# Performance work log

Hardware: AMD Instinct MI355X
Metric: run time of the kernel (lower is better)

The kernel has to match this reference:

```python
import jax, jax.numpy as jnp
import numpy as np
from jax import lax

NAMES = ['k', 'v', 'q', 'eta', 'alpha', 'memory']
RES = {'k': True, 'v': True, 'q': True, 'eta': False, 'alpha': False, 'memory': True}
CHUNK = 16


def _mlp(x, st, residual):
    # x: (B,C,d_in); st W1:(B,d_out,d_hid) W2:(B,d_hid,d_in) b1:(B,d_out) b2:(B,d_hid)
    h = jax.nn.silu(jnp.einsum('bcd,bhd->bch', x, st['W2']) + st['b2'][:, None, :])
    out = jnp.einsum('bch,boh->bco', h, st['W1']) + st['b1'][:, None, :]
    return x + out if residual else out


def _dgd_grads(x, target, st, residual):
    # manual chain rule for L = (1/2C)||M(x)-target||^2
    C = x.shape[1]
    pre = jnp.einsum('bcd,bhd->bch', x, st['W2']) + st['b2'][:, None, :]
    sig = jax.nn.sigmoid(pre)
    h = pre * sig  # silu
    pred = jnp.einsum('bch,boh->bco', h, st['W1']) + st['b1'][:, None, :]
    if residual:
        pred = x + pred
    error = (pred - target) / C  # (B,C,d_out)
    dW1 = jnp.einsum('bco,bch->boh', error, h)
    db1 = error.sum(axis=1)
    dl_dh = jnp.einsum('bco,boh->bch', error, st['W1'])
    silu_grad = sig * (1.0 + pre * (1.0 - sig))
    dl_dpre = dl_dh * silu_grad
    dW2 = jnp.einsum('bch,bcd->bhd', dl_dpre, x)
    db2 = dl_dpre.sum(axis=1)
    return {'W1': dW1, 'W2': dW2, 'b1': db1, 'b2': db2}


def _clamp(w):
    B = w.shape[0]
    flat = w.reshape(B, -1)
    norm = jnp.linalg.norm(flat, axis=1)
    max_n = np.sqrt(flat.shape[1]).astype(np.float32)
    scale = jnp.minimum(max_n / (norm + 1e-8), 1.0)
    return w * scale.reshape((B,) + (1,) * (w.ndim - 1))


def _l2norm(x):
    return x / jnp.maximum(jnp.linalg.norm(x, axis=-1, keepdims=True), 1e-12)


def _titans(x, mods, in_W, in_b, out_W, out_b, ln_g, ln_b):
    B, T, _ = x.shape
    C = CHUNK
    NC = T // C
    z = x @ in_W.T + in_b  # (B,T,d_memory)
    zc = z.reshape(B, NC, C, -1).transpose(1, 0, 2, 3)  # (NC,B,C,d)

    states = {}
    for name in NAMES:
        W1, b1, W2, b2 = mods[name]
        states[name] = {
            'W1': jnp.broadcast_to(W1, (B,) + W1.shape),
            'b1': jnp.broadcast_to(b1, (B,) + b1.shape),
            'W2': jnp.broadcast_to(W2, (B,) + W2.shape),
            'b2': jnp.broadcast_to(b2, (B,) + b2.shape),
        }

    def step(st, z_chunk):
        k = _mlp(z_chunk, st['k'], True)
        v = _mlp(z_chunk, st['v'], True)
        q = _mlp(z_chunk, st['q'], True)
        eta = jax.nn.sigmoid(_mlp(z_chunk, st['eta'], False))    # (B,C,1)
        alpha = jax.nn.sigmoid(_mlp(z_chunk, st['alpha'], False))
        k = _l2norm(k)
        q = _l2norm(q)
        o = _mlp(q, st['memory'], True)
        ea = eta.mean(axis=1)    # (B,1)
        aa = alpha.mean(axis=1)  # (B,1)
        new = {}
        for name in NAMES:
            s = st[name]
            res = RES[name]
            v_hat = lax.stop_gradient(_mlp(v, s, res))
            g = _dgd_grads(k, v_hat, s, res)
            ns = {}
            for pn in ('W1', 'W2', 'b1', 'b2'):
                gr = g[pn]
                a = aa.reshape((aa.shape[0],) + (1,) * (gr.ndim - 1))
                e = ea.reshape((ea.shape[0],) + (1,) * (gr.ndim - 1))
                ns[pn] = _clamp(a * s[pn] - e * gr)
            new[name] = ns
        new = jax.tree.map(lax.stop_gradient, new)  # bptt_depth=0 detach
        return new, o

    _, outs = lax.scan(step, states, zc)  # outs: (NC,B,C,d)
    out = outs.transpose(1, 0, 2, 3).reshape(B, T, -1)
    mu = out.mean(axis=-1, keepdims=True)
    var = out.var(axis=-1, keepdims=True)
    out = (out - mu) / jnp.sqrt(var + 1e-5) * ln_g + ln_b
    return out @ out_W.T + out_b


def setup_inputs() -> dict:
    key = jax.random.key(0)
    B, T, Dm = 4, 2048, 1024
    Dmem = 1024
    ks = jax.random.split(key, 10)
    inp = {'x': jax.random.normal(ks[0], (B, T, Dm), jnp.float32)}
    d_outs = {'k': Dmem, 'v': Dmem, 'q': Dmem, 'eta': 1, 'alpha': 1, 'memory': Dmem}
    b1_special = {'eta': -3.0, 'alpha': 3.0}
    for i, (m, do) in enumerate(d_outs.items()):
        inp[f'{m}_W1'] = jnp.zeros((do, Dmem), jnp.float32)
        inp[f'{m}_b1'] = jnp.full((do,), b1_special.get(m, 0.0), jnp.float32)
        inp[f'{m}_W2'] = (jax.random.normal(ks[1 + i], (Dmem, Dm), jnp.float32)
                          * np.sqrt(2.0 / Dm).astype(np.float32))
        inp[f'{m}_b2'] = jnp.zeros((Dmem,), jnp.float32)
    inp['in_W'] = jax.random.normal(ks[7], (Dmem, Dm), jnp.float32) * 0.02
    inp['in_b'] = jnp.zeros((Dmem,), jnp.float32)
    inp['out_W'] = jax.random.normal(ks[8], (Dm, Dmem), jnp.float32) * 0.02
    inp['out_b'] = jnp.zeros((Dm,), jnp.float32)
    inp['ln_g'] = jnp.ones((Dmem,), jnp.float32)
    inp['ln_b'] = jnp.zeros((Dmem,), jnp.float32)
    return inp


def reference(x, k_W1, k_b1, k_W2, k_b2, v_W1, v_b1, v_W2, v_b2,
              q_W1, q_b1, q_W2, q_b2, eta_W1, eta_b1, eta_W2, eta_b2,
              alpha_W1, alpha_b1, alpha_W2, alpha_b2,
              memory_W1, memory_b1, memory_W2, memory_b2,
              in_W, in_b, out_W, out_b, ln_g, ln_b):
    mods = {
        'k': (k_W1, k_b1, k_W2, k_b2),
        'v': (v_W1, v_b1, v_W2, v_b2),
        'q': (q_W1, q_b1, q_W2, q_b2),
        'eta': (eta_W1, eta_b1, eta_W2, eta_b2),
        'alpha': (alpha_W1, alpha_b1, alpha_W2, alpha_b2),
        'memory': (memory_W1, memory_b1, memory_W2, memory_b2),
    }
    return _titans(x, mods, in_W, in_b, out_W, out_b, ln_g, ln_b)
```

## Files before the change

### kernel.cpp

```cpp
#include <hip/hip_runtime.h>
#include <math.h>

#define DI __device__ __forceinline__

namespace {

typedef unsigned short u16;
typedef unsigned int u32;
typedef __attribute__((ext_vector_type(8))) short bf8;
typedef __attribute__((ext_vector_type(4))) float f4;

DI f4 MFB(bf8 a, bf8 b, f4 c) { return __builtin_amdgcn_mfma_f32_16x16x32_bf16(a, b, c, 0, 0, 0); }

constexpr int DOUTS[6] = {1024, 1024, 1024, 1, 1, 1024};
constexpr int BIGM[4] = {0, 1, 2, 5};

constexpr long SZ_BIGM = 2100224, SZ_SMALLM = 1051648;
constexpr long MODOFF[6] = {0, SZ_BIGM, 2 * SZ_BIGM, 3 * SZ_BIGM,
                            3 * SZ_BIGM + SZ_SMALLM, 3 * SZ_BIGM + 2 * SZ_SMALLM};
constexpr long BSTRIDE = 3 * SZ_BIGM + 2 * SZ_SMALLM + SZ_BIGM;

constexpr long OFF_Z     = 0;
constexpr long OFF_STATE = 8388608;
constexpr long OFF_SPRE5 = OFF_STATE + 4 * BSTRIDE;
// ... 37 lines not shown
}

DI void sumsqReduce(float ss, float* slack, float* dst) {
#pragma unroll
  for (int st = 32; st >= 1; st >>= 1) ss += __shfl_xor(ss, st);
  const int tid = threadIdx.x;
  if ((tid & 63) == 0) slack[tid >> 6] = ss;
  __syncthreads();
  if (tid == 0) atomicAdd(dst, slack[0] + slack[1] + slack[2] + slack[3]);
  __syncthreads();
}

DI void split3v(const float v[8], bf8& p0, bf8& p1, bf8& p2) {
#pragma unroll
  for (int i = 0; i < 8; i++) {
    const u32 u = __float_as_uint(v[i]);
    const float f0 = __uint_as_float(u & 0xffff0000u);
    const float r1 = v[i] - f0;
    const u32 u1 = __float_as_uint(r1);
    const float f1 = __uint_as_float(u1 & 0xffff0000u);
    const float r2 = r1 - f1;
    p0[i] = (short)(u >> 16);
    p1[i] = (short)(u1 >> 16);
    p2[i] = (short)f2bf(r2);
  }
}
DI void split3p(const float* p, bf8& p0, bf8& p1, bf8& p2) {
  const float4 a = *(const float4*)p, b = *(const float4*)(p + 4);
  const float v[8] = {a.x, a.y, a.z, a.w, b.x, b.y, b.z, b.w};
  split3v(v, p0, p1, p2);
}

__global__ void k_probe(float* ws) {
  const int l = threadIdx.x, cl = l & 15, kq = l >> 4;
  bf8 af, bf_;
#pragma unroll
  for (int i = 0; i < 8; i++) { af[i] = 0; bf_[i] = 0; }
  if (kq == 0) {
    af[0] = (short)f2bf((float)(cl + 1));
    bf_[0] = (short)f2bf((float)(128 * (cl + 1)));
  }
  f4 d = MFB(af, bf_, f4{0.f, 0.f, 0.f, 0.f});
  bool m0 = true, m1 = true;
#pragma unroll
  for (int r = 0; r < 4; r++) {
    m0 = m0 && (d[r] == (float)((kq * 4 + r + 1) * 128 * (cl + 1)));
    m1 = m1 && (d[r] == (float)((cl + 1) * 128 * (kq * 4 + r + 1)));
  }
  const unsigned long long b0 = __ballot(m0), b1 = __ballot(m1);
  if (l == 0) ws[OFF_FLAG] = (b0 == ~0ull) ? 0.f : ((b1 == ~0ull) ? 1.f : 0.f);
}

template <class EF>
DI void mcK1(float* sm, const float* __restrict__ X, const float* W,
             int n0, int flg, EF&& ef) {
  const int tid = threadIdx.x, g = tid >> 6, l = tid & 63, cl = l & 15, kq = l >> 4;
  f4 a0 = {0.f, 0.f, 0.f, 0.f}, a1 = {0.f, 0.f, 0.f, 0.f};
  const float* Xr = X + (long)cl * 1024 + g * 256 + kq * 8;
  const float* Wr0 = W + (long)(n0 + cl) * 1024 + g * 256 + kq * 8;
  const float* Wr1 = Wr0 + 16 * 1024;
#pragma unroll 2
  for (int ch = 0; ch < 8; ch++) {
    bf8 x0, x1, x2, w0, w1, w2;
    split3p(Xr + ch * 32, x0, x1, x2);
    split3p(Wr0 + ch * 32, w0, w1, w2);
    a0 = MFB(x2, w0, a0); a0 = MFB(x1, w1, a0); a0 = MFB(x0, w2, a0);
    a0 = MFB(x1, w0, a0); a0 = MFB(x0, w1, a0); a0 = MFB(x0, w0, a0);
    split3p(Wr1 + ch * 32, w0, w1, w2);
    a1 = MFB(x2, w0, a1); a1 = MFB(x1, w1, a1); a1 = MFB(x0, w2, a1);
    a1 = MFB(x1, w0, a1); a1 = MFB(x0, w1, a1); a1 = MFB(x0, w0, a1);
  }
  *(f4*)(sm + g * 256 + l * 4) = a0;
  *(f4*)(sm + 1024 + g * 256 + l * 4) = a1;
  __syncthreads();
  const int le = tid >> 2, re = tid & 3;
  const int ccl = le & 15, ckq = le >> 4;
  const int c = flg ? ccl : ckq * 4 + re;
  const int nb = flg ? ckq * 4 + re : ccl;
#pragma unroll
  for (int half = 0; half < 2; half++) {
    const float v = sm[half * 1024 + le * 4 + re] + sm[half * 1024 + 256 + le * 4 + re] +
                    sm[half * 1024 + 512 + le * 4 + re] + sm[half * 1024 + 768 + le * 4 + re];
    ef(c, n0 + half * 16 + nb, v);
  }
}

template <class EF>
DI void mcK2(float* sm, const float* __restrict__ X1, const float* __restrict__ X2,
             const float* W, int n0, int flg, EF&& ef) {
  const int tid = threadIdx.x, g = tid >> 6, l = tid & 63, cl = l & 15, kq = l >> 4;
  f4 a10 = {0.f, 0.f, 0.f, 0.f}, a11 = {0.f, 0.f, 0.f, 0.f};
  f4 a20 = {0.f, 0.f, 0.f, 0.f}, a21 = {0.f, 0.f, 0.f, 0.f};
  const float* X1r = X1 + (long)cl * 1024 + g * 256 + kq * 8;
  const float* X2r = X2 + (long)cl * 1024 + g * 256 + kq * 8;
  const float* Wr0 = W + (long)(n0 + cl) * 1024 + g * 256 + kq * 8;
  const float* Wr1 = Wr0 + 16 * 1024;
#pragma unroll 2
  for (int ch = 0; ch < 8; ch++) {
    bf8 x0, x1, x2, y0, y1, y2, w0, w1, w2;
    split3p(X1r + ch * 32, x0, x1, x2);
    split3p(X2r + ch * 32, y0, y1, y2);
    split3p(Wr0 + ch * 32, w0, w1, w2);
    a10 = MFB(x2, w0, a10); a10 = MFB(x1, w1, a10); a10 = MFB(x0, w2, a10);
    a10 = MFB(x1, w0, a10); a10 = MFB(x0, w1, a10); a10 = MFB(x0, w0, a10);
    a20 = MFB(y2, w0, a20); a20 = MFB(y1, w1, a20); a20 = MFB(y0, w2, a20);
    a20 = MFB(y1, w0, a20); a20 = MFB(y0, w1, a20); a20 = MFB(y0, w0, a20);
    split3p(Wr1 + ch * 32, w0, w1, w2);
    a11 = MFB(x2, w0, a11); a11 = MFB(x1, w1, a11); a11 = MFB(x0, w2, a11);
    a11 = MFB(x1, w0, a11); a11 = MFB(x0, w1, a11); a11 = MFB(x0, w0, a11);
    a21 = MFB(y2, w0, a21); a21 = MFB(y1, w1, a21); a21 = MFB(y0, w2, a21);
    a21 = MFB(y1, w0, a21); a21 = MFB(y0, w1, a21); a21 = MFB(y0, w0, a21);
  }
  *(f4*)(sm + g * 256 + l * 4) = a10;
  *(f4*)(sm + 1024 + g * 256 + l * 4) = a11;
  *(f4*)(sm + 2048 + g * 256 + l * 4) = a20;
  *(f4*)(sm + 3072 + g * 256 + l * 4) = a21;
  __syncthreads();
  const int le = tid >> 2, re = tid & 3;
  const int ccl = le & 15, ckq = le >> 4;
  const int c = flg ? ccl : ckq * 4 + re;
  const int nb = flg ? ckq * 4 + re : ccl;
#pragma unroll
  for (int half = 0; half < 2; half++) {
    const int o1 = half * 1024 + le * 4 + re, o2 = 2048 + half * 1024 + le * 4 + re;
    const float v1 = sm[o1] + sm[o1 + 256] + sm[o1 + 512] + sm[o1 + 768];
    const float v2 = sm[o2] + sm[o2 + 256] + sm[o2 + 512] + sm[o2 + 768];
    ef(c, n0 + half * 16 + nb, v1, v2);
  }
}

template <class EF>
DI void mcK1t(float* sm, const float* __restrict__ E, const float* W1,
              int h0, int flg, EF&& ef) {
  const int tid = threadIdx.x, g = tid >> 6, l = tid & 63, cl = l & 15, kq = l >> 4;
  f4 a0 = {0.f, 0.f, 0.f, 0.f}, a1 = {0.f, 0.f, 0.f, 0.f};
  const float* Er = E + (long)cl * 1024 + g * 256 + kq * 8;
  const float* Wc0 = W1 + (long)(g * 256 + kq * 8) * 1024 + h0 + cl;
  const float* Wc1 = Wc0 + 16;
#pragma unroll 2
  for (int ch = 0; ch < 8; ch++) {
    bf8 x0, x1, x2, w0, w1, w2;
    split3p(Er + ch * 32, x0, x1, x2);
    float v[8];
#pragma unroll
    for (int i = 0; i < 8; i++) v[i] = Wc0[(long)(ch * 32 + i) * 1024];
    split3v(v, w0, w1, w2);
    a0 = MFB(x2, w0, a0); a0 = MFB(x1, w1, a0); a0 = MFB(x0, w2, a0);
    a0 = MFB(x1, w0, a0); a0 = MFB(x0, w1, a0); a0 = MFB(x0, w0, a0);
#pragma unroll
    for (int i = 0; i < 8; i++) v[i] = Wc1[(long)(ch * 32 + i) * 1024];
    split3v(v, w0, w1, w2);
    a1 = MFB(x2, w0, a1); a1 = MFB(x1, w1, a1); a1 = MFB(x0, w2, a1);
    a1 = MFB(x1, w0, a1); a1 = MFB(x0, w1, a1); a1 = MFB(x0, w0, a1);
  }
  *(f4*)(sm + g * 256 + l * 4) = a0;
  *(f4*)(sm + 1024 + g * 256 + l * 4) = a1;
  __syncthreads();
  const int le = tid >> 2, re = tid & 3;
  const int ccl = le & 15, ckq = le >> 4;
  const int c = flg ? ccl : ckq * 4 + re;
  const int hb = flg ? ckq * 4 + re : ccl;
#pragma unroll
  for (int half = 0; half < 2; half++) {
    const float v = sm[half * 1024 + le * 4 + re] + sm[half * 1024 + 256 + le * 4 + re] +
                    sm[half * 1024 + 512 + le * 4 + re] + sm[half * 1024 + 768 + le * 4 + re];
    ef(c, h0 + half * 16 + hb, v);
  }
}


__global__ __launch_bounds__(256) void k_p0(float* ws, InPtrs in) {
  const long i = threadIdx.x + (long)blockIdx.x * 256;
  if (i < 256) { ws[OFF_RSSQ + i] = 0.f; return; }
  if (i < 448) { ws[OFF_SUMSQ + (i - 256)] = 0.f; return; }
  if (i < 456) { ws[OFF_EA + (i - 448)] = 0.f; return; }
  const long j = i - 456;
  if (j < 24 * 2048) {
    const int bm = (int)(j >> 11), q = (int)(j & 2047);
    const int b = bm / 6, m = bm % 6;
    float* vc = vecp(modBase(ws, b, m), m);
    if (q < 1024) { if (q < DOUTS[m]) vc[q] = in.p[2 + 4 * m][q]; }
    else vc[1024 + (q - 1024)] = in.p[4 + 4 * m][q - 1024];
    return;
  }
  const long j2 = j - 49152;
  if (j2 < 8192) {
    const int e = (int)(j2 >> 10), b = e >> 1, m = 3 + (e & 1);
    const int h = (int)(j2 & 1023);
    vecp(modBase(ws, b, m), m)[2048 + h] = in.p[1 + 4 * m][h];
  }
}

__global__ __launch_bounds__(256) void k_pc(float* ws, InPtrs in) {
  const int bid = blockIdx.x, job = bid >> 9, sub = bid & 511;
  const long e0 = (long)sub * 2048 + threadIdx.x * 8;
  int m; bool w1;
  if (job < 6) { m = job; w1 = false; }
  else { m = BIGM[job - 6]; w1 = true; }
  const float* src = in.p[(w1 ? 1 : 3) + 4 * m];
  const float4 a = *(const float4*)(src + e0);
  const float4 b4 = *(const float4*)(src + e0 + 4);
#pragma unroll
  for (int q = 0; q < 4; q++) {
    float* dst = modBase(ws, q, m) + (w1 ? 1048576 : 0);
    *(float4*)(dst + e0) = a;
    *(float4*)(dst + e0 + 4) = b4;
  }
}

__global__ __launch_bounds__(256) void k_gbig(const float* __restrict__ X,
                                              const float* A,
                                              const float* __restrict__ bias,
                                              float* __restrict__ Y,
                                              const float* flagp) {
  __shared__ float sm[2048];
  const int bid = blockIdx.x, nb = bid & 31;
  const long rb = bid >> 5;
  const int flg = (int)flagp[0];
  const float* Xr = X + rb * 16 * 1024;
  float* Yr = Y + rb * 16 * 1024;
  mcK1(sm, Xr, A, nb * 32, flg, [&](int c, int n, float v) {
    Yr[(long)c * 1024 + n] = v + bias[n];
  });
}


__global__ __launch_bounds__(256) void k_s1(float* ws, int t) {
  __shared__ float sm[2048];
  const int bid = blockIdx.x, tid = threadIdx.x;
  if (bid == 640) {
    const int pc = t & 1;
    if (tid < 128) ws[OFF_RSSQ + pc * 128 + tid] = 0.f;
    else if (tid < 224) ws[OFF_SUMSQ + pc * 96 + (tid - 128)] = 0.f;
    return;
  }
  const int n0 = (bid & 31) * 32, m = (bid >> 5) % 5, b = bid / 160;
  const int flg = (int)ws[OFF_FLAG];
  const int sp = (t + 1) & 1;
  const float* zc = ws + OFF_Z + ((long)b * 2048 + (long)t * 16) * 1024;
  float* base = modBase(ws, b, m);
  const float cW2 = sclOf(ws, sp, b, m, 2), cb2 = sclOf(ws, sp, b, m, 3);
  const float* b2v = vecp(base, m) + 1024;
  float* Y = ws + OFF_SPRE5 + ((long)b * 5 + m) * 16384;
  mcK1(sm, zc, base, n0, flg, [&](int c, int n, float v) {
    Y[(long)c * 1024 + n] = silu(fmaf(cW2, v, cb2 * b2v[n]));
  });
}

__global__ __launch_bounds__(256) void k_s2(float* ws, int t) {
  __shared__ float sm[2048 + 16 + 64];
  float* smr = sm + 2048;
  float* sm2 = sm + 2064;
  const int tid = threadIdx.x, bid = blockIdx.x;
  const int sp = (t + 1) & 1, pc = t & 1;
  if (bid < 384) {
    const int n0 = (bid & 31) * 32, m = (bid >> 5) % 3, b = bid / 96;
    const int flg = (int)ws[OFF_FLAG];
    if (tid < 16) smr[tid] = 0.f;
    const float* spre = ws + OFF_SPRE5 + ((long)b * 5 + m) * 16384;
    float* base = modBase(ws, b, m);
    const float* zc = ws + OFF_Z + ((long)b * 2048 + (long)t * 16) * 1024;
    const float cW1 = sclOf(ws, sp, b, m, 0), cb1 = sclOf(ws, sp, b, m, 1);
    const float* b1v = vecp(base, m);
    float* out = ws + OFF_KVQ + ((long)b * 3 + m) * 16384;
    const bool sq = (m != 1);
    mcK1(sm, spre, base + 1048576, n0, flg, [&](int c, int n, float v) {
      const float val = fmaf(cW1, v, fmaf(cb1, b1v[n], zc[(long)c * 1024 + n]));
      out[(long)c * 1024 + n] = val;
      if (sq) atomicAdd(&smr[c], val * val);
    });
    __syncthreads();
    if (sq && tid < 16)
      atomicAdd(ws + OFF_RSSQ + pc * 128 + (long)b * 32 + (m == 0 ? 0 : 16) + tid,
                smr[tid]);
  } else {
    const int e = bid - 384, b = e >> 1, m = 3 + (e & 1);
    const float* spre = ws + OFF_SPRE5 + ((long)b * 5 + m) * 16384;
    float* base = modBase(ws, b, m);
    const float* w1 = vecp(base, m) + 2048;
    float av[16];
#pragma unroll
    for (int c = 0; c < 16; c++) av[c] = 0.f;
    for (int jj = 0; jj < 4; jj++) {
      const int h = tid + 256 * jj;
      const float w = w1[h];
#pragma unroll
      for (int c = 0; c < 16; c++) av[c] = fmaf(spre[c * 1024 + h], w, av[c]);
    }
#pragma unroll
    for (int st = 1; st < 64; st <<= 1)
#pragma unroll
      for (int c = 0; c < 16; c++) av[c] += __shfl_xor(av[c], st);
    if ((tid & 63) == 0) {
      const int w4 = tid >> 6;
#pragma unroll
      for (int c = 0; c < 16; c++) sm2[w4 * 16 + c] = av[c];
    }
    __syncthreads();
    if (tid == 0) {
      const float cW1 = sclOf(ws, sp, b, m, 0), cb1 = sclOf(ws, sp, b, m, 1);
      const float b10 = vecp(base, m)[0];
      float s = 0.f;
      for (int c = 0; c < 16; c++) {
        const float tot = sm2[c] + sm2[16 + c] + sm2[32 + c] + sm2[48 + c];
        s += sigm(fmaf(cW1, tot, cb1 * b10));
      }
      ws[OFF_EA + ((m == 3) ? 0 : 4) + b] = s * 0.0625f;
    }
  }
}

__global__ __launch_bounds__(256) void k_s3(float* ws, int t) {
  __shared__ float sm[4096 + 16];
  float* sminv = sm + 4096;
  const int bid = blockIdx.x, tid = threadIdx.x;
  const int flg = (int)ws[OFF_FLAG];
  const int sp = (t + 1) & 1, pc = t & 1;
  if (bid < 768) {
    const int n0 = (bid & 31) * 32, m = (bid >> 5) % 6, b = bid / 192;
    if (tid < 16)
      sminv[tid] = 1.f / fmaxf(sqrtf(ws[OFF_RSSQ + pc * 128 + (long)b * 32 + tid]), 1e-12f);
    const float* vX = ws + OFF_KVQ + ((long)b * 3 + 1) * 16384;
    const float* kX = ws + OFF_KVQ + ((long)b * 3 + 0) * 16384;
    float* base = modBase(ws, b, m);
    const float cW2 = sclOf(ws, sp, b, m, 2), cb2 = sclOf(ws, sp, b, m, 3);
    const float* b2v = vecp(base, m) + 1024;
    float* Ysv = ws + OFF_SPREV + ((long)b * 6 + m) * 16384;
    float* Yk = ws + OFF_PREK + ((long)b * 6 + m) * 16384;
    float* Ysk = ws + OFF_SPREK + ((long)b * 6 + m) * 16384;
    mcK2(sm, vX, kX, base, n0, flg, [&](int c, int n, float v1, float v2) {
      const float bb = cb2 * b2v[n];
      Ysv[(long)c * 1024 + n] = silu(fmaf(cW2, v1, bb));
      const float pk = fmaf(cW2 * sminv[c], v2, bb);
      Yk[(long)c * 1024 + n] = pk;
      Ysk[(long)c * 1024 + n] = silu(pk);
    });
  } else {
    const int id = bid - 768, n0 = (id & 31) * 32, b = id >> 5;
    if (tid < 16)
      sminv[tid] = 1.f / fmaxf(sqrtf(ws[OFF_RSSQ + pc * 128 + (long)b * 32 + 16 + tid]), 1e-12f);
    const float* qX = ws + OFF_KVQ + ((long)b * 3 + 2) * 16384;
    float* base = modBase(ws, b, 5);
    const float cW2 = sclOf(ws, sp, b, 5, 2), cb2 = sclOf(ws, sp, b, 5, 3);
    const float* b2v = vecp(base, 5) + 1024;
    float* Y = ws + OFF_SPREO + (long)b * 16384;
    mcK1(sm, qX, base, n0, flg, [&](int c, int n, float v) {
      Y[(long)c * 1024 + n] = silu(fmaf(cW2 * sminv[c], v, cb2 * b2v[n]));
    });
  }
}

__global__ __launch_bounds__(256) void k_s4(float* ws, int t) {
  __shared__ float sm[4096 + 16 + 128];
  float* sminv = sm + 4096;
  float* sm4 = sm + 4112;
  const int tid = threadIdx.x, bid = blockIdx.x;
  const int sp = (t + 1) & 1, pc = t & 1;
  if (bid < 512) {
    const int n0 = (bid & 31) * 32, mi = (bid >> 5) & 3, b = bid >> 7;
    const int m = BIGM[mi];
    const int flg = (int)ws[OFF_FLAG];
    if (tid < 16)
      sminv[tid] = 1.f / fmaxf(sqrtf(ws[OFF_RSSQ + pc * 128 + (long)b * 32 + tid]), 1e-12f);
    const float* sprev = ws + OFF_SPREV + ((long)b * 6 + m) * 16384;
    const float* sprek = ws + OFF_SPREK + ((long)b * 6 + m) * 16384;
    float* base = modBase(ws, b, m);
    const float cW1 = sclOf(ws, sp, b, m, 0), cb1 = sclOf(ws, sp, b, m, 1);
    const float* b1v = vecp(base, m);
    const float* vraw = ws + OFF_KVQ + ((long)b * 3 + 1) * 16384;
    const float* kraw = ws + OFF_KVQ + ((long)b * 3 + 0) * 16384;
    float* errP = ws + OFF_ERR + ((long)b * 6 + m) * 16384;
    mcK2(sm, sprev, sprek, base + 1048576, n0, flg, [&](int c, int n, float v1, float v2) {
      const float bbb = cb1 * b1v[n];
      const float vh = fmaf(cW1, v1, bbb + vraw[(long)c * 1024 + n]);
      const float pr = fmaf(cW1, v2, bbb + kraw[(long)c * 1024 + n] * sminv[c]);
      errP[(long)c * 1024 + n] = (pr - vh) * 0.0625f;
    });
  } else if (bid < 640) {
    const int id = bid - 512, n0 = (id & 31) * 32, b = id >> 5;
    const int flg = (int)ws[OFF_FLAG];
    if (tid < 16)
      sminv[tid] = 1.f / fmaxf(sqrtf(ws[OFF_RSSQ + pc * 128 + (long)b * 32 + 16 + tid]), 1e-12f);
    const float* spreo = ws + OFF_SPREO + (long)b * 16384;
    float* base = modBase(ws, b, 5);
    const float cW1 = sclOf(ws, sp, b, 5, 0), cb1 = sclOf(ws, sp, b, 5, 1);
    const float* b1v = vecp(base, 5);
    const float* qraw = ws + OFF_KVQ + ((long)b * 3 + 2) * 16384;
    float* zc = ws + OFF_Z + ((long)b * 2048 + (long)t * 16) * 1024;
    mcK1(sm, spreo, base + 1048576, n0, flg, [&](int c, int n, float v) {
      zc[(long)c * 1024 + n] = fmaf(cW1, v, cb1 * b1v[n] + qraw[(long)c * 1024 + n] * sminv[c]);
    });
  } else {
    const int id = bid - 640, b = id >> 1, m = 3 + (id & 1);
    const float* sprev = ws + OFF_SPREV + ((long)b * 6 + m) * 16384;
    const float* sprek = ws + OFF_SPREK + ((long)b * 6 + m) * 16384;
    float* base = modBase(ws, b, m);
    const float* w1 = vecp(base, m) + 2048;
    float av[16], ap[16];
#pragma unroll
    for (int c = 0; c < 16; c++) { av[c] = 0.f; ap[c] = 0.f; }
    for (int jj = 0; jj < 4; jj++) {
      const int h = tid + 256 * jj;
      const float w = w1[h];
#pragma unroll
      for (int c = 0; c < 16; c++) {
        av[c] = fmaf(sprev[c * 1024 + h], w, av[c]);
        ap[c] = fmaf(sprek[c * 1024 + h], w, ap[c]);
      }
    }
#pragma unroll
    for (int st = 1; st < 64; st <<= 1)
#pragma unroll
      for (int c = 0; c < 16; c++) {
        av[c] += __shfl_xor(av[c], st);
        ap[c] += __shfl_xor(ap[c], st);
      }
    if ((tid & 63) == 0) {
      const int w4 = tid >> 6;
#pragma unroll
      for (int c = 0; c < 16; c++) { sm4[w4 * 32 + c] = av[c]; sm4[w4 * 32 + 16 + c] = ap[c]; }
    }
    __syncthreads();
    if (tid == 0) {
      const float cW1 = sclOf(ws, sp, b, m, 0), cb1 = sclOf(ws, sp, b, m, 1);
      const float b10 = vecp(base, m)[0];
      float* errP = ws + OFF_ERR + ((long)b * 6 + m) * 16384;
      for (int c = 0; c < 16; c++) {
        const float sv = sm4[c] + sm4[32 + c] + sm4[64 + c] + sm4[96 + c];
        const float sp2 = sm4[16 + c] + sm4[48 + c] + sm4[80 + c] + sm4[112 + c];
        errP[c * 1024] = (fmaf(cW1, sp2, cb1 * b10) - fmaf(cW1, sv, cb1 * b10)) * 0.0625f;
      }
    }
  }
}

__global__ __launch_bounds__(256) void k_s5(float* ws, int t) {
  __shared__ float sm[2048];
  const int tid = threadIdx.x, bid = blockIdx.x;
  const int sp = (t + 1) & 1;
  if (bid < 512) {
    const int h0 = (bid & 31) * 32, mi = (bid >> 5) & 3, b = bid >> 7;
    const int m = BIGM[mi];
    const int flg = (int)ws[OFF_FLAG];
    float* base = modBase(ws, b, m);
    const float* errP = ws + OFF_ERR + ((long)b * 6 + m) * 16384;
    const float cW1 = sclOf(ws, sp, b, m, 0);
    const float* prek = ws + OFF_PREK + ((long)b * 6 + m) * 16384;
    float* dlp = ws + OFF_DLP + ((long)b * 6 + m) * 16384;
    mcK1t(sm, errP, base + 1048576, h0, flg, [&](int c, int h, float v) {
      const float pre = prek[(long)c * 1024 + h];
      const float sg = sigm(pre);
      dlp[(long)c * 1024 + h] = cW1 * v * (sg * (1.f + pre * (1.f - sg)));
    });
  } else {
    const int e = bid - 512, sub = e & 3, bm = e >> 2, b = bm >> 1, m = 3 + (bm & 1);
    const float cW1 = sclOf(ws, sp, b, m, 0);
    const float* errP = ws + OFF_ERR + ((long)b * 6 + m) * 16384;
    const float* prek = ws + OFF_PREK + ((long)b * 6 + m) * 16384;
    const float* w1 = vecp(modBase(ws, b, m), m) + 2048;
    float* dlp = ws + OFF_DLP + ((long)b * 6 + m) * 16384;
    for (int i = tid; i < 4096; i += 256) {
      const long idx = (long)sub * 4096 + i;
      const int c = (int)(idx >> 10), h = (int)(idx & 1023);
      const float pre = prek[idx];
      const float sg = sigm(pre);
      dlp[idx] = errP[c * 1024] * cW1 * w1[h] * (sg * (1.f + pre * (1.f - sg)));
    }
  }
}

__global__ __launch_bounds__(256) void k_s6(float* ws, int t) {
  __shared__ float sm[64 * 20 + 8];
  float* slack = sm + 64 * 20;
  const int tid = threadIdx.x, bid = blockIdx.x;
  const int sp = (t + 1) & 1, pc = t & 1;
  if (bid < 640) {
    const bool isW2 = bid < 384;
    int b, m, r0, pslot;
    float* W;
    float4 fac[16];
    const float* tsrc;
    if (isW2) {
      const int bm = bid >> 4;
      b = bm / 6; m = bm % 6; r0 = (bid & 15) * 64;
      W = modBase(ws, b, m);
      pslot = 2;
      tsrc = ws + OFF_DLP + ((long)b * 6 + m) * 16384;
      const float* kraw = ws + OFF_KVQ + ((long)b * 3) * 16384;
#pragma unroll
      for (int c = 0; c < 16; c++) {
        const float inv = 1.f / fmaxf(sqrtf(ws[OFF_RSSQ + pc * 128 + (long)b * 32 + c]), 1e-12f);
        const float4 kk = *(const float4*)(kraw + (long)c * 1024 + tid * 4);
        fac[c].x = kk.x * inv; fac[c].y = kk.y * inv;
        fac[c].z = kk.z * inv; fac[c].w = kk.w * inv;
      }
    } else {
      const int id = bid - 384, bm = id >> 4;
      b = bm >> 2; m = BIGM[bm & 3]; r0 = (id & 15) * 64;
      W = modBase(ws, b, m) + 1048576;
      pslot = 0;
      tsrc = ws + OFF_ERR + ((long)b * 6 + m) * 16384;
      const float* sprek = ws + OFF_SPREK + ((long)b * 6 + m) * 16384;
#pragma unroll
      for (int c = 0; c < 16; c++)
        fac[c] = *(const float4*)(sprek + (long)c * 1024 + tid * 4);
    }
    for (int f = tid; f < 1024; f += 256) {
      const int c = f >> 6, hh = f & 63;
      sm[hh * 20 + c] = tsrc[(long)c * 1024 + r0 + hh];
    }
    __syncthreads();
    const float ea = ws[OFF_EA + b], aa = ws[OFF_EA + 4 + b];
    const float ac = aa * sclOf(ws, sp, b, m, pslot);
    float ss = 0.f;
// ... 66 lines not shown
    for (int h = tid; h < 1024; h += 256) {
      float gs = 0.f;
#pragma unroll
      for (int c = 0; c < 16; c++)
        gs = fmaf(errP[c * 1024], sprek[c * 1024 + h], gs);
      const float nw = fmaf(ac, vc[2048 + h], -ea * gs);
      vc[2048 + h] = nw;
      ss = fmaf(nw, nw, ss);
    }
    sumsqReduce(ss, slack, ws + OFF_SUMSQ + pc * 96 + sidx(b, m, 0));
  }
}


__global__ __launch_bounds__(256) void k_ln(float* ws, const float* __restrict__ g,
                                            const float* __restrict__ bb) {
  __shared__ float sm[8];
  float* p = ws + OFF_Z + (long)blockIdx.x * 1024;
  const int tid = threadIdx.x;
  float s = 0.f, s2 = 0.f;
  for (int j = tid; j < 1024; j += 256) {
    const float v = p[j];
    s += v;
    s2 = fmaf(v, v, s2);
  }
#pragma unroll
  for (int st = 32; st >= 1; st >>= 1) { s += __shfl_xor(s, st); s2 += __shfl_xor(s2, st); }
  if ((tid & 63) == 0) { sm[tid >> 6] = s; sm[4 + (tid >> 6)] = s2; }
  __syncthreads();
  const float S = sm[0] + sm[1] + sm[2] + sm[3];
  const float S2 = sm[4] + sm[5] + sm[6] + sm[7];
  const float mu = S * (1.f / 1024.f);
  const float var = S2 * (1.f / 1024.f) - mu * mu;
  const float inv = 1.f / sqrtf(var + 1e-5f);
  for (int j = tid; j < 1024; j += 256) {
    p[j] = fmaf((p[j] - mu) * inv, g[j], bb[j]);
  }
}

}

extern "C" void kernel_launch(void* const* d_in, const int* in_sizes, int n_in,
                              void* d_out, int out_size, void* d_ws, size_t ws_size,
                              hipStream_t stream) {
  (void)in_sizes; (void)n_in; (void)out_size;
  if (ws_size < (size_t)WS_FLOATS * sizeof(float)) return;
  float* ws = (float*)d_ws;
  InPtrs ip;
  for (int i = 0; i < 31; i++) ip.p[i] = (const float*)d_in[i];

  k_probe<<<1, 64, 0, stream>>>(ws);
  k_p0<<<256, 256, 0, stream>>>(ws, ip);
  k_pc<<<5120, 256, 0, stream>>>(ws, ip);
  k_gbig<<<16384, 256, 0, stream>>>((const float*)d_in[0], (const float*)d_in[25],
                                    (const float*)d_in[26], ws + OFF_Z, ws + OFF_FLAG);

  for (int t = 0; t < 128; t++) {
    k_s1<<<641, 256, 0, stream>>>(ws, t);
    k_s2<<<392, 256, 0, stream>>>(ws, t);
    k_s3<<<896, 256, 0, stream>>>(ws, t);
    k_s4<<<648, 256, 0, stream>>>(ws, t);
    k_s5<<<544, 256, 0, stream>>>(ws, t);
    k_s6<<<696, 256, 0, stream>>>(ws, t);
  }

  k_ln<<<8192, 256, 0, stream>>>(ws, (const float*)d_in[29], (const float*)d_in[30]);
  k_gbig<<<16384, 256, 0, stream>>>(ws + OFF_Z, (const float*)d_in[27],
                                    (const float*)d_in[28], (float*)d_out, ws + OFF_FLAG);
}
```

Measured before the change: 21.89 ms.

## Widen per-step GEMM tiles to 64 columns with 512-thread split-K blocks

```diff
diff --git a/kernel.cpp b/kernel.cpp
--- a/kernel.cpp
+++ b/kernel.cpp
@@ -113,8 +113,135 @@
 }
 
 template <class EF>
-DI void mcK1(float* sm, const float* __restrict__ X, const float* W,
-             int n0, int flg, EF&& ef) {
+DI void mcK1w(float* sm, const float* __restrict__ X, const float* W,
+              int n0, int flg, EF&& ef) {
+  const int tid = threadIdx.x, g = tid >> 6, l = tid & 63, cl = l & 15, kq = l >> 4;
+  f4 acc[4];
+#pragma unroll
+  for (int s = 0; s < 4; s++) acc[s] = f4{0.f, 0.f, 0.f, 0.f};
+  const float* Xr = X + (long)cl * 1024 + g * 128 + kq * 8;
+  const float* Wr = W + (long)(n0 + cl) * 1024 + g * 128 + kq * 8;
+#pragma unroll 2
+  for (int ch = 0; ch < 4; ch++) {
+    bf8 x0, x1, x2;
+    split3p(Xr + ch * 32, x0, x1, x2);
+#pragma unroll
+    for (int s = 0; s < 4; s++) {
+      bf8 w0, w1, w2;
+      split3p(Wr + (long)s * 16384 + ch * 32, w0, w1, w2);
+      acc[s] = MFB(x2, w0, acc[s]); acc[s] = MFB(x1, w1, acc[s]); acc[s] = MFB(x0, w2, acc[s]);
+      acc[s] = MFB(x1, w0, acc[s]); acc[s] = MFB(x0, w1, acc[s]); acc[s] = MFB(x0, w0, acc[s]);
+    }
+  }
+#pragma unroll
+  for (int s = 0; s < 4; s++) *(f4*)(sm + (g * 4 + s) * 256 + l * 4) = acc[s];
+  __syncthreads();
+#pragma unroll
+  for (int i = 0; i < 2; i++) {
+    const int idx = tid * 2 + i, s = idx >> 8, pos = idx & 255;
+    float v = 0.f;
+#pragma unroll
+    for (int gg = 0; gg < 8; gg++) v += sm[(gg * 4 + s) * 256 + pos];
+    const int le = pos >> 2, re = pos & 3;
+    const int ccl = le & 15, ckq = le >> 4;
+    const int c = flg ? ccl : ckq * 4 + re;
+    const int nb = flg ? ckq * 4 + re : ccl;
+    ef(c, n0 + s * 16 + nb, v);
+  }
+}
+
+template <class EF>
+DI void mcK2w(float* sm, const float* __restrict__ X1, const float* __restrict__ X2,
+              const float* W, int n0, int flg, EF&& ef) {
+  const int tid = threadIdx.x, g = tid >> 6, l = tid & 63, cl = l & 15, kq = l >> 4;
+  f4 a1[4], a2[4];
+#pragma unroll
+  for (int s = 0; s < 4; s++) { a1[s] = f4{0.f, 0.f, 0.f, 0.f}; a2[s] = f4{0.f, 0.f, 0.f, 0.f}; }
+  const float* X1r = X1 + (long)cl * 1024 + g * 128 + kq * 8;
+  const float* X2r = X2 + (long)cl * 1024 + g * 128 + kq * 8;
+  const float* Wr = W + (long)(n0 + cl) * 1024 + g * 128 + kq * 8;
+#pragma unroll 2
+  for (int ch = 0; ch < 4; ch++) {
+    bf8 x0, x1, x2, y0, y1, y2;
+    split3p(X1r + ch * 32, x0, x1, x2);
+    split3p(X2r + ch * 32, y0, y1, y2);
+#pragma unroll
+    for (int s = 0; s < 4; s++) {
+      bf8 w0, w1, w2;
+      split3p(Wr + (long)s * 16384 + ch * 32, w0, w1, w2);
+      a1[s] = MFB(x2, w0, a1[s]); a1[s] = MFB(x1, w1, a1[s]); a1[s] = MFB(x0, w2, a1[s]);
+      a1[s] = MFB(x1, w0, a1[s]); a1[s] = MFB(x0, w1, a1[s]); a1[s] = MFB(x0, w0, a1[s]);
+      a2[s] = MFB(y2, w0, a2[s]); a2[s] = MFB(y1, w1, a2[s]); a2[s] = MFB(y0, w2, a2[s]);
+      a2[s] = MFB(y1, w0, a2[s]); a2[s] = MFB(y0, w1, a2[s]); a2[s] = MFB(y0, w0, a2[s]);
+    }
+  }
+#pragma unroll
+  for (int s = 0; s < 4; s++) {
+    *(f4*)(sm + (g * 4 + s) * 256 + l * 4) = a1[s];
+    *(f4*)(sm + 8192 + (g * 4 + s) * 256 + l * 4) = a2[s];
+  }
+  __syncthreads();
+#pragma unroll
+  for (int i = 0; i < 2; i++) {
+    const int idx = tid * 2 + i, s = idx >> 8, pos = idx & 255;
+    float v1 = 0.f, v2 = 0.f;
+#pragma unroll
+    for (int gg = 0; gg < 8; gg++) {
+      v1 += sm[(gg * 4 + s) * 256 + pos];
+      v2 += sm[8192 + (gg * 4 + s) * 256 + pos];
+    }
+    const int le = pos >> 2, re = pos & 3;
+    const int ccl = le & 15, ckq = le >> 4;
+    const int c = flg ? ccl : ckq * 4 + re;
+    const int nb = flg ? ckq * 4 + re : ccl;
+    ef(c, n0 + s * 16 + nb, v1, v2);
+  }
+}
+
+template <class EF>
+DI void mcK1tw(float* sm, const float* __restrict__ E, const float* W1,
+               int h0, int flg, EF&& ef) {
+  const int tid = threadIdx.x, g = tid >> 6, l = tid & 63, cl = l & 15, kq = l >> 4;
+  f4 acc[4];
+#pragma unroll
+  for (int s = 0; s < 4; s++) acc[s] = f4{0.f, 0.f, 0.f, 0.f};
+  const float* Er = E + (long)cl * 1024 + g * 128 + kq * 8;
+  const float* Wc = W1 + (long)(g * 128 + kq * 8) * 1024 + h0 + cl;
+#pragma unroll 2
+  for (int ch = 0; ch < 4; ch++) {
+    bf8 x0, x1, x2;
+    split3p(Er + ch * 32, x0, x1, x2);
+#pragma unroll
+    for (int s = 0; s < 4; s++) {
+      float v[8];
+#pragma unroll
+      for (int i = 0; i < 8; i++) v[i] = Wc[(long)(ch * 32 + i) * 1024 + s * 16];
+      bf8 w0, w1, w2;
+      split3v(v, w0, w1, w2);
+      acc[s] = MFB(x2, w0, acc[s]); acc[s] = MFB(x1, w1, acc[s]); acc[s] = MFB(x0, w2, acc[s]);
+      acc[s] = MFB(x1, w0, acc[s]); acc[s] = MFB(x0, w1, acc[s]); acc[s] = MFB(x0, w0, acc[s]);
+    }
+  }
+#pragma unroll
+  for (int s = 0; s < 4; s++) *(f4*)(sm + (g * 4 + s) * 256 + l * 4) = acc[s];
+  __syncthreads();
+#pragma unroll
+  for (int i = 0; i < 2; i++) {
+    const int idx = tid * 2 + i, s = idx >> 8, pos = idx & 255;
+    float v = 0.f;
+#pragma unroll
+    for (int gg = 0; gg < 8; gg++) v += sm[(gg * 4 + s) * 256 + pos];
+    const int le = pos >> 2, re = pos & 3;
+    const int ccl = le & 15, ckq = le >> 4;
+    const int c = flg ? ccl : ckq * 4 + re;
+    const int hb = flg ? ckq * 4 + re : ccl;
+    ef(c, h0 + s * 16 + hb, v);
+  }
+}
+
+template <class EF>
+DI void mcK1o(float* sm, const float* __restrict__ X, const float* W,
+              int n0, int flg, EF&& ef) {
   const int tid = threadIdx.x, g = tid >> 6, l = tid & 63, cl = l & 15, kq = l >> 4;
   f4 a0 = {0.f, 0.f, 0.f, 0.f}, a1 = {0.f, 0.f, 0.f, 0.f};
   const float* Xr = X + (long)cl * 1024 + g * 256 + kq * 8;
@@ -146,89 +273,6 @@
   }
 }
 
-template <class EF>
-DI void mcK2(float* sm, const float* __restrict__ X1, const float* __restrict__ X2,
-             const float* W, int n0, int flg, EF&& ef) {
-  const int tid = threadIdx.x, g = tid >> 6, l = tid & 63, cl = l & 15, kq = l >> 4;
-  f4 a10 = {0.f, 0.f, 0.f, 0.f}, a11 = {0.f, 0.f, 0.f, 0.f};
-  f4 a20 = {0.f, 0.f, 0.f, 0.f}, a21 = {0.f, 0.f, 0.f, 0.f};
-  const float* X1r = X1 + (long)cl * 1024 + g * 256 + kq * 8;
-  const float* X2r = X2 + (long)cl * 1024 + g * 256 + kq * 8;
-  const float* Wr0 = W + (long)(n0 + cl) * 1024 + g * 256 + kq * 8;
-  const float* Wr1 = Wr0 + 16 * 1024;
-#pragma unroll 2
-  for (int ch = 0; ch < 8; ch++) {
-    bf8 x0, x1, x2, y0, y1, y2, w0, w1, w2;
-    split3p(X1r + ch * 32, x0, x1, x2);
-    split3p(X2r + ch * 32, y0, y1, y2);
-    split3p(Wr0 + ch * 32, w0, w1, w2);
-    a10 = MFB(x2, w0, a10); a10 = MFB(x1, w1, a10); a10 = MFB(x0, w2, a10);
-    a10 = MFB(x1, w0, a10); a10 = MFB(x0, w1, a10); a10 = MFB(x0, w0, a10);
-    a20 = MFB(y2, w0, a20); a20 = MFB(y1, w1, a20); a20 = MFB(y0, w2, a20);
-    a20 = MFB(y1, w0, a20); a20 = MFB(y0, w1, a20); a20 = MFB(y0, w0, a20);
-    split3p(Wr1 + ch * 32, w0, w1, w2);
-    a11 = MFB(x2, w0, a11); a11 = MFB(x1, w1, a11); a11 = MFB(x0, w2, a11);
-    a11 = MFB(x1, w0, a11); a11 = MFB(x0, w1, a11); a11 = MFB(x0, w0, a11);
-    a21 = MFB(y2, w0, a21); a21 = MFB(y1, w1, a21); a21 = MFB(y0, w2, a21);
-    a21 = MFB(y1, w0, a21); a21 = MFB(y0, w1, a21); a21 = MFB(y0, w0, a21);
-  }
-  *(f4*)(sm + g * 256 + l * 4) = a10;
-  *(f4*)(sm + 1024 + g * 256 + l * 4) = a11;
-  *(f4*)(sm + 2048 + g * 256 + l * 4) = a20;
-  *(f4*)(sm + 3072 + g * 256 + l * 4) = a21;
-  __syncthreads();
-  const int le = tid >> 2, re = tid & 3;
-  const int ccl = le & 15, ckq = le >> 4;
-  const int c = flg ? ccl : ckq * 4 + re;
-  const int nb = flg ? ckq * 4 + re : ccl;
-#pragma unroll
-  for (int half = 0; half < 2; half++) {
-    const int o1 = half * 1024 + le * 4 + re, o2 = 2048 + half * 1024 + le * 4 + re;
-    const float v1 = sm[o1] + sm[o1 + 256] + sm[o1 + 512] + sm[o1 + 768];
-    const float v2 = sm[o2] + sm[o2 + 256] + sm[o2 + 512] + sm[o2 + 768];
-    ef(c, n0 + half * 16 + nb, v1, v2);
-  }
-}
-
-template <class EF>
-DI void mcK1t(float* sm, const float* __restrict__ E, const float* W1,
-              int h0, int flg, EF&& ef) {
-  const int tid = threadIdx.x, g = tid >> 6, l = tid & 63, cl = l & 15, kq = l >> 4;
-  f4 a0 = {0.f, 0.f, 0.f, 0.f}, a1 = {0.f, 0.f, 0.f, 0.f};
-  const float* Er = E + (long)cl * 1024 + g * 256 + kq * 8;
-  const float* Wc0 = W1 + (long)(g * 256 + kq * 8) * 1024 + h0 + cl;
-  const float* Wc1 = Wc0 + 16;
-#pragma unroll 2
-  for (int ch = 0; ch < 8; ch++) {
-    bf8 x0, x1, x2, w0, w1, w2;
-    split3p(Er + ch * 32, x0, x1, x2);
-    float v[8];
-#pragma unroll
-    for (int i = 0; i < 8; i++) v[i] = Wc0[(long)(ch * 32 + i) * 1024];
-    split3v(v, w0, w1, w2);
-    a0 = MFB(x2, w0, a0); a0 = MFB(x1, w1, a0); a0 = MFB(x0, w2, a0);
-    a0 = MFB(x1, w0, a0); a0 = MFB(x0, w1, a0); a0 = MFB(x0, w0, a0);
-#pragma unroll
-    for (int i = 0; i < 8; i++) v[i] = Wc1[(long)(ch * 32 + i) * 1024];
-    split3v(v, w0, w1, w2);
-    a1 = MFB(x2, w0, a1); a1 = MFB(x1, w1, a1); a1 = MFB(x0, w2, a1);
-    a1 = MFB(x1, w0, a1); a1 = MFB(x0, w1, a1); a1 = MFB(x0, w0, a1);
-  }
-  *(f4*)(sm + g * 256 + l * 4) = a0;
-  *(f4*)(sm + 1024 + g * 256 + l * 4) = a1;
-  __syncthreads();
-  const int le = tid >> 2, re = tid & 3;
-  const int ccl = le & 15, ckq = le >> 4;
-  const int c = flg ? ccl : ckq * 4 + re;
-  const int hb = flg ? ckq * 4 + re : ccl;
-#pragma unroll
-  for (int half = 0; half < 2; half++) {
-    const float v = sm[half * 1024 + le * 4 + re] + sm[half * 1024 + 256 + le * 4 + re] +
-                    sm[half * 1024 + 512 + le * 4 + re] + sm[half * 1024 + 768 + le * 4 + re];
-    ef(c, h0 + half * 16 + hb, v);
-  }
-}
-
 
 __global__ __launch_bounds__(256) void k_p0(float* ws, InPtrs in) {
   const long i = threadIdx.x + (long)blockIdx.x * 256;
@@ -269,33 +313,55 @@
   }
 }
 
-__global__ __launch_bounds__(256) void k_gbig(const float* __restrict__ X,
-                                              const float* A,
-                                              const float* __restrict__ bias,
-                                              float* __restrict__ Y,
-                                              const float* flagp) {
-  __shared__ float sm[2048];
-  const int bid = blockIdx.x, nb = bid & 31;
-  const long rb = bid >> 5;
+__global__ __launch_bounds__(512) void k_gbig2(const float* __restrict__ X,
+                                               const float* A,
+                                               const float* __restrict__ bias,
+                                               float* __restrict__ Y,
+                                               const float* flagp) {
+  const int bid = blockIdx.x, nb = bid & 15;
+  const long rbg = bid >> 4;
+  const int tid = threadIdx.x, g = tid >> 6, l = tid & 63, cl = l & 15, kq = l >> 4;
   const int flg = (int)flagp[0];
-  const float* Xr = X + rb * 16 * 1024;
-  float* Yr = Y + rb * 16 * 1024;
-  mcK1(sm, Xr, A, nb * 32, flg, [&](int c, int n, float v) {
-    Yr[(long)c * 1024 + n] = v + bias[n];
-  });
-}
-
-
-__global__ __launch_bounds__(256) void k_s1(float* ws, int t) {
-  __shared__ float sm[2048];
+  const int n0 = nb * 64;
+  const long row0 = rbg * 128 + g * 16;
+  f4 acc[4];
+#pragma unroll
+  for (int s = 0; s < 4; s++) acc[s] = f4{0.f, 0.f, 0.f, 0.f};
+  const float* Xr = X + (row0 + cl) * 1024 + kq * 8;
+  const float* Wr = A + (long)(n0 + cl) * 1024 + kq * 8;
+#pragma unroll 2
+  for (int ch = 0; ch < 32; ch++) {
+    bf8 x0, x1, x2;
+    split3p(Xr + ch * 32, x0, x1, x2);
+#pragma unroll
+    for (int s = 0; s < 4; s++) {
+      bf8 w0, w1, w2;
+      split3p(Wr + (long)s * 16384 + ch * 32, w0, w1, w2);
+      acc[s] = MFB(x2, w0, acc[s]); acc[s] = MFB(x1, w1, acc[s]); acc[s] = MFB(x0, w2, acc[s]);
+      acc[s] = MFB(x1, w0, acc[s]); acc[s] = MFB(x0, w1, acc[s]); acc[s] = MFB(x0, w0, acc[s]);
+    }
+  }
+#pragma unroll
+  for (int s = 0; s < 4; s++)
+#pragma unroll
+    for (int r = 0; r < 4; r++) {
+      const int c = flg ? cl : kq * 4 + r;
+      const int n = n0 + s * 16 + (flg ? kq * 4 + r : cl);
+      Y[(row0 + c) * 1024 + n] = acc[s][r] + bias[n];
+    }
+}
+
+
+__global__ __launch_bounds__(512) void k_s1(float* ws, int t) {
+  __shared__ float sm[8192];
   const int bid = blockIdx.x, tid = threadIdx.x;
-  if (bid == 640) {
+  if (bid == 320) {
     const int pc = t & 1;
     if (tid < 128) ws[OFF_RSSQ + pc * 128 + tid] = 0.f;
     else if (tid < 224) ws[OFF_SUMSQ + pc * 96 + (tid - 128)] = 0.f;
     return;
   }
-  const int n0 = (bid & 31) * 32, m = (bid >> 5) % 5, b = bid / 160;
+  const int n0 = (bid & 15) * 64, m = (bid >> 4) % 5, b = bid / 80;
   const int flg = (int)ws[OFF_FLAG];
   const int sp = (t + 1) & 1;
   const float* zc = ws + OFF_Z + ((long)b * 2048 + (long)t * 16) * 1024;
@@ -303,7 +369,7 @@
   const float cW2 = sclOf(ws, sp, b, m, 2), cb2 = sclOf(ws, sp, b, m, 3);
   const float* b2v = vecp(base, m) + 1024;
   float* Y = ws + OFF_SPRE5 + ((long)b * 5 + m) * 16384;
-  mcK1(sm, zc, base, n0, flg, [&](int c, int n, float v) {
+  mcK1w(sm, zc, base, n0, flg, [&](int c, int n, float v) {
     Y[(long)c * 1024 + n] = silu(fmaf(cW2, v, cb2 * b2v[n]));
   });
 }
@@ -325,7 +391,7 @@
     const float* b1v = vecp(base, m);
     float* out = ws + OFF_KVQ + ((long)b * 3 + m) * 16384;
     const bool sq = (m != 1);
-    mcK1(sm, spre, base + 1048576, n0, flg, [&](int c, int n, float v) {
+    mcK1o(sm, spre, base + 1048576, n0, flg, [&](int c, int n, float v) {
       const float val = fmaf(cW1, v, fmaf(cb1, b1v[n], zc[(long)c * 1024 + n]));
       out[(long)c * 1024 + n] = val;
       if (sq) atomicAdd(&smr[c], val * val);
@@ -371,14 +437,14 @@
   }
 }
 
-__global__ __launch_bounds__(256) void k_s3(float* ws, int t) {
-  __shared__ float sm[4096 + 16];
-  float* sminv = sm + 4096;
+__global__ __launch_bounds__(512) void k_s3(float* ws, int t) {
+  __shared__ float sm[16384 + 16];
+  float* sminv = sm + 16384;
   const int bid = blockIdx.x, tid = threadIdx.x;
   const int flg = (int)ws[OFF_FLAG];
   const int sp = (t + 1) & 1, pc = t & 1;
-  if (bid < 768) {
-    const int n0 = (bid & 31) * 32, m = (bid >> 5) % 6, b = bid / 192;
+  if (bid < 384) {
+    const int n0 = (bid & 15) * 64, m = (bid >> 4) % 6, b = bid / 96;
     if (tid < 16)
       sminv[tid] = 1.f / fmaxf(sqrtf(ws[OFF_RSSQ + pc * 128 + (long)b * 32 + tid]), 1e-12f);
     const float* vX = ws + OFF_KVQ + ((long)b * 3 + 1) * 16384;
@@ -389,7 +455,7 @@
     float* Ysv = ws + OFF_SPREV + ((long)b * 6 + m) * 16384;
     float* Yk = ws + OFF_PREK + ((long)b * 6 + m) * 16384;
     float* Ysk = ws + OFF_SPREK + ((long)b * 6 + m) * 16384;
-    mcK2(sm, vX, kX, base, n0, flg, [&](int c, int n, float v1, float v2) {
+    mcK2w(sm, vX, kX, base, n0, flg, [&](int c, int n, float v1, float v2) {
       const float bb = cb2 * b2v[n];
       Ysv[(long)c * 1024 + n] = silu(fmaf(cW2, v1, bb));
       const float pk = fmaf(cW2 * sminv[c], v2, bb);
@@ -397,7 +463,7 @@
       Ysk[(long)c * 1024 + n] = silu(pk);
     });
   } else {
-    const int id = bid - 768, n0 = (id & 31) * 32, b = id >> 5;
+    const int id = bid - 384, n0 = (id & 15) * 64, b = id >> 4;
     if (tid < 16)
       sminv[tid] = 1.f / fmaxf(sqrtf(ws[OFF_RSSQ + pc * 128 + (long)b * 32 + 16 + tid]), 1e-12f);
     const float* qX = ws + OFF_KVQ + ((long)b * 3 + 2) * 16384;
@@ -405,20 +471,20 @@
     const float cW2 = sclOf(ws, sp, b, 5, 2), cb2 = sclOf(ws, sp, b, 5, 3);
     const float* b2v = vecp(base, 5) + 1024;
     float* Y = ws + OFF_SPREO + (long)b * 16384;
-    mcK1(sm, qX, base, n0, flg, [&](int c, int n, float v) {
+    mcK1w(sm, qX, base, n0, flg, [&](int c, int n, float v) {
       Y[(long)c * 1024 + n] = silu(fmaf(cW2 * sminv[c], v, cb2 * b2v[n]));
     });
   }
 }
 
-__global__ __launch_bounds__(256) void k_s4(float* ws, int t) {
-  __shared__ float sm[4096 + 16 + 128];
-  float* sminv = sm + 4096;
-  float* sm4 = sm + 4112;
+__global__ __launch_bounds__(512) void k_s4(float* ws, int t) {
+  __shared__ float sm[16384 + 16 + 256];
+  float* sminv = sm + 16384;
+  float* sm4 = sm + 16400;
   const int tid = threadIdx.x, bid = blockIdx.x;
   const int sp = (t + 1) & 1, pc = t & 1;
-  if (bid < 512) {
-    const int n0 = (bid & 31) * 32, mi = (bid >> 5) & 3, b = bid >> 7;
+  if (bid < 256) {
+    const int n0 = (bid & 15) * 64, mi = (bid >> 4) & 3, b = bid >> 6;
     const int m = BIGM[mi];
     const int flg = (int)ws[OFF_FLAG];
     if (tid < 16)
@@ -431,14 +497,14 @@
     const float* vraw = ws + OFF_KVQ + ((long)b * 3 + 1) * 16384;
     const float* kraw = ws + OFF_KVQ + ((long)b * 3 + 0) * 16384;
     float* errP = ws + OFF_ERR + ((long)b * 6 + m) * 16384;
-    mcK2(sm, sprev, sprek, base + 1048576, n0, flg, [&](int c, int n, float v1, float v2) {
+    mcK2w(sm, sprev, sprek, base + 1048576, n0, flg, [&](int c, int n, float v1, float v2) {
       const float bbb = cb1 * b1v[n];
       const float vh = fmaf(cW1, v1, bbb + vraw[(long)c * 1024 + n]);
       const float pr = fmaf(cW1, v2, bbb + kraw[(long)c * 1024 + n] * sminv[c]);
       errP[(long)c * 1024 + n] = (pr - vh) * 0.0625f;
     });
-  } else if (bid < 640) {
-    const int id = bid - 512, n0 = (id & 31) * 32, b = id >> 5;
+  } else if (bid < 320) {
+    const int id = bid - 256, n0 = (id & 15) * 64, b = id >> 4;
     const int flg = (int)ws[OFF_FLAG];
     if (tid < 16)
       sminv[tid] = 1.f / fmaxf(sqrtf(ws[OFF_RSSQ + pc * 128 + (long)b * 32 + 16 + tid]), 1e-12f);
@@ -448,11 +514,11 @@
     const float* b1v = vecp(base, 5);
     const float* qraw = ws + OFF_KVQ + ((long)b * 3 + 2) * 16384;
     float* zc = ws + OFF_Z + ((long)b * 2048 + (long)t * 16) * 1024;
-    mcK1(sm, spreo, base + 1048576, n0, flg, [&](int c, int n, float v) {
+    mcK1w(sm, spreo, base + 1048576, n0, flg, [&](int c, int n, float v) {
       zc[(long)c * 1024 + n] = fmaf(cW1, v, cb1 * b1v[n] + qraw[(long)c * 1024 + n] * sminv[c]);
     });
   } else {
-    const int id = bid - 640, b = id >> 1, m = 3 + (id & 1);
+    const int id = bid - 320, b = id >> 1, m = 3 + (id & 1);
     const float* sprev = ws + OFF_SPREV + ((long)b * 6 + m) * 16384;
     const float* sprek = ws + OFF_SPREK + ((long)b * 6 + m) * 16384;
     float* base = modBase(ws, b, m);
@@ -460,8 +526,8 @@
     float av[16], ap[16];
 #pragma unroll
     for (int c = 0; c < 16; c++) { av[c] = 0.f; ap[c] = 0.f; }
-    for (int jj = 0; jj < 4; jj++) {
-      const int h = tid + 256 * jj;
+    for (int jj = 0; jj < 2; jj++) {
+      const int h = tid + 512 * jj;
       const float w = w1[h];
 #pragma unroll
       for (int c = 0; c < 16; c++) {
@@ -477,9 +543,9 @@
         ap[c] += __shfl_xor(ap[c], st);
       }
     if ((tid & 63) == 0) {
-      const int w4 = tid >> 6;
-#pragma unroll
-      for (int c = 0; c < 16; c++) { sm4[w4 * 32 + c] = av[c]; sm4[w4 * 32 + 16 + c] = ap[c]; }
+      const int w8 = tid >> 6;
+#pragma unroll
+      for (int c = 0; c < 16; c++) { sm4[w8 * 32 + c] = av[c]; sm4[w8 * 32 + 16 + c] = ap[c]; }
     }
     __syncthreads();
     if (tid == 0) {
@@ -487,20 +553,20 @@
       const float b10 = vecp(base, m)[0];
       float* errP = ws + OFF_ERR + ((long)b * 6 + m) * 16384;
       for (int c = 0; c < 16; c++) {
-        const float sv = sm4[c] + sm4[32 + c] + sm4[64 + c] + sm4[96 + c];
-        const float sp2 = sm4[16 + c] + sm4[48 + c] + sm4[80 + c] + sm4[112 + c];
+        float sv = 0.f, sp2 = 0.f;
+        for (int w8 = 0; w8 < 8; w8++) { sv += sm4[w8 * 32 + c]; sp2 += sm4[w8 * 32 + 16 + c]; }
         errP[c * 1024] = (fmaf(cW1, sp2, cb1 * b10) - fmaf(cW1, sv, cb1 * b10)) * 0.0625f;
       }
     }
   }
 }
 
-__global__ __launch_bounds__(256) void k_s5(float* ws, int t) {
-  __shared__ float sm[2048];
+__global__ __launch_bounds__(512) void k_s5(float* ws, int t) {
+  __shared__ float sm[8192];
   const int tid = threadIdx.x, bid = blockIdx.x;
   const int sp = (t + 1) & 1;
-  if (bid < 512) {
-    const int h0 = (bid & 31) * 32, mi = (bid >> 5) & 3, b = bid >> 7;
+  if (bid < 256) {
+    const int h0 = (bid & 15) * 64, mi = (bid >> 4) & 3, b = bid >> 6;
     const int m = BIGM[mi];
     const int flg = (int)ws[OFF_FLAG];
     float* base = modBase(ws, b, m);
@@ -508,19 +574,19 @@
     const float cW1 = sclOf(ws, sp, b, m, 0);
     const float* prek = ws + OFF_PREK + ((long)b * 6 + m) * 16384;
     float* dlp = ws + OFF_DLP + ((long)b * 6 + m) * 16384;
-    mcK1t(sm, errP, base + 1048576, h0, flg, [&](int c, int h, float v) {
+    mcK1tw(sm, errP, base + 1048576, h0, flg, [&](int c, int h, float v) {
       const float pre = prek[(long)c * 1024 + h];
       const float sg = sigm(pre);
       dlp[(long)c * 1024 + h] = cW1 * v * (sg * (1.f + pre * (1.f - sg)));
     });
   } else {
-    const int e = bid - 512, sub = e & 3, bm = e >> 2, b = bm >> 1, m = 3 + (bm & 1);
+    const int e = bid - 256, sub = e & 3, bm = e >> 2, b = bm >> 1, m = 3 + (bm & 1);
     const float cW1 = sclOf(ws, sp, b, m, 0);
     const float* errP = ws + OFF_ERR + ((long)b * 6 + m) * 16384;
     const float* prek = ws + OFF_PREK + ((long)b * 6 + m) * 16384;
     const float* w1 = vecp(modBase(ws, b, m), m) + 2048;
     float* dlp = ws + OFF_DLP + ((long)b * 6 + m) * 16384;
-    for (int i = tid; i < 4096; i += 256) {
+    for (int i = tid; i < 4096; i += 512) {
       const long idx = (long)sub * 4096 + i;
       const int c = (int)(idx >> 10), h = (int)(idx & 1023);
       const float pre = prek[idx];
@@ -693,19 +759,19 @@
   k_probe<<<1, 64, 0, stream>>>(ws);
   k_p0<<<256, 256, 0, stream>>>(ws, ip);
   k_pc<<<5120, 256, 0, stream>>>(ws, ip);
-  k_gbig<<<16384, 256, 0, stream>>>((const float*)d_in[0], (const float*)d_in[25],
+  k_gbig2<<<1024, 512, 0, stream>>>((const float*)d_in[0], (const float*)d_in[25],
                                     (const float*)d_in[26], ws + OFF_Z, ws + OFF_FLAG);
 
   for (int t = 0; t < 128; t++) {
-    k_s1<<<641, 256, 0, stream>>>(ws, t);
+    k_s1<<<321, 512, 0, stream>>>(ws, t);
     k_s2<<<392, 256, 0, stream>>>(ws, t);
-    k_s3<<<896, 256, 0, stream>>>(ws, t);
-    k_s4<<<648, 256, 0, stream>>>(ws, t);
-    k_s5<<<544, 256, 0, stream>>>(ws, t);
+    k_s3<<<448, 512, 0, stream>>>(ws, t);
+    k_s4<<<328, 512, 0, stream>>>(ws, t);
+    k_s5<<<288, 512, 0, stream>>>(ws, t);
     k_s6<<<696, 256, 0, stream>>>(ws, t);
   }
 
   k_ln<<<8192, 256, 0, stream>>>(ws, (const float*)d_in[29], (const float*)d_in[30]);
-  k_gbig<<<16384, 256, 0, stream>>>(ws + OFF_Z, (const float*)d_in[27],
+  k_gbig2<<<1024, 512, 0, stream>>>(ws + OFF_Z, (const float*)d_in[27],
                                     (const float*)d_in[28], (float*)d_out, ws + OFF_FLAG);
 }
```

Result: faster. 20.63 ms (-5.8%).
